# Optimization experiments

Measured on AMD Instinct MI355X. Metric: run time of the kernel, lower is better.

The kernel has to match this reference:

```python
import jax, jax.numpy as jnp
import numpy as np
from functools import partial

B = 1024          # batch of VRP instances
N_CUST = 100      # customers
N = N_CUST + 1    # nodes incl. depot (node 0)
E = 128           # embed_dim
H = 8             # n_heads
DH = E // H       # head depth
CLIP = 10.0
T = 2 * N         # fixed number of decode steps (env.n_nodes * 2)


def setup_inputs() -> dict:
    key = jax.random.key(0)
    ks = jax.random.split(key, 11)
    s = E ** -0.5
    return {
        "depot_xy": jax.random.uniform(ks[0], (B, 2), dtype=jnp.float32),
        "customer_xy": jax.random.uniform(ks[1], (B, N_CUST, 2), dtype=jnp.float32),
        # demands normalized by vehicle capacity (1..9 / 50 for VRP100)
        "demand": jax.random.uniform(ks[2], (B, N_CUST), dtype=jnp.float32, minval=0.02, maxval=0.18),
        "node_embeddings": jax.random.normal(ks[3], (B, N, E), dtype=jnp.float32),
        "graph_embedding": jax.random.normal(ks[4], (B, E), dtype=jnp.float32),
        "Wk1": jax.random.normal(ks[5], (E, E), dtype=jnp.float32) * s,
        "Wv": jax.random.normal(ks[6], (E, E), dtype=jnp.float32) * s,
        "Wk2": jax.random.normal(ks[7], (E, E), dtype=jnp.float32) * s,
        "Wq_fixed": jax.random.normal(ks[8], (E, E), dtype=jnp.float32) * s,
        "Wout": jax.random.normal(ks[9], (E, E), dtype=jnp.float32) * s,
        "Wq_step": jax.random.normal(ks[10], (E + 1, E), dtype=jnp.float32) * s,
    }


def _decode(depot_xy, customer_xy, demand, node_embeddings, graph_embedding,
            Wk1, Wv, Wk2, Wq_fixed, Wout, Wq_step):
    # ---- compute_static ----
    Q_fixed = jnp.einsum('be,ef->bf', graph_embedding, Wq_fixed)[:, None, :]  # [B,1,E]
    K1 = jnp.einsum('bne,ef->bnf', node_embeddings, Wk1)                      # [B,N,E]
    V  = jnp.einsum('bne,ef->bnf', node_embeddings, Wv)
    K2 = jnp.einsum('bne,ef->bnf', node_embeddings, Wk2)
    K1h = K1.reshape(B, N, H, DH)
    Vh  = V.reshape(B, N, H, DH)
    inv_sqrt_dh = 1.0 / np.sqrt(DH)
    inv_sqrt_e = 1.0 / np.sqrt(E)
    bidx = jnp.arange(B)
    NEG = jnp.float32(-1e9)

    def step(carry, _):
        mask, D, prev_node, visited = carry
        # step_context = [embedding of current node, remaining capacity D]
        prev_emb = node_embeddings[bidx, prev_node]                 # [B,E]
        step_context = jnp.concatenate([prev_emb, D], axis=-1)[:, None, :]  # [B,1,E+1]
        # ---- compute_dynamic ----
        Q1 = Q_fixed + jnp.einsum('bqc,cf->bqf', step_context, Wq_step)      # [B,1,E]
        Q1h = Q1.reshape(B, 1, H, DH)
        scores = jnp.einsum('bqhd,bkhd->bhqk', Q1h, K1h) * inv_sqrt_dh       # [B,H,1,N]
        scores = jnp.where(mask[:, None, None, :], NEG, scores)
        attn = jax.nn.softmax(scores, axis=-1)
        glimpse = jnp.einsum('bhqk,bkhd->bqhd', attn, Vh).reshape(B, 1, E)
        Q2 = jnp.einsum('bqe,ef->bqf', glimpse, Wout)                        # [B,1,E]
        logits = CLIP * jnp.tanh(jnp.einsum('bqe,bke->bqk', Q2, K2) * inv_sqrt_e)
        logits = jnp.where(mask[:, None, :], NEG, logits)[:, 0]             # [B,N]
        log_p = jax.nn.log_softmax(logits, axis=-1)
        next_node = jnp.argmax(log_p, axis=-1)                               # greedy decode
        # ---- env._get_step ----
        is_depot = next_node == 0
        cust = jnp.clip(next_node - 1, 0, N_CUST - 1)
        sel_dem = jnp.where(is_depot, 0.0, demand[bidx, cust])
        D_new = jnp.where(is_depot[:, None], 1.0, D - sel_dem[:, None])      # refill at depot
        sel_onehot = (jnp.arange(N_CUST)[None, :] == cust[:, None]) & (~is_depot[:, None])
        visited = visited | sel_onehot
        mask_cust = visited | (demand > D_new)                               # visited or too big
        all_visited = jnp.all(visited, axis=-1)
        mask_depot = is_depot & (~all_visited)                               # can't stay at depot
        mask = jnp.concatenate([mask_depot[:, None], mask_cust], axis=-1)
        return (mask, D_new, next_node, visited), (log_p, next_node)

    mask0 = jnp.concatenate([jnp.ones((B, 1), bool), jnp.zeros((B, N_CUST), bool)], axis=-1)
    D0 = jnp.ones((B, 1), jnp.float32)
    prev0 = jnp.zeros((B,), jnp.int32)
    visited0 = jnp.zeros((B, N_CUST), bool)
    _, (log_ps, tours) = jax.lax.scan(step, (mask0, D0, prev0, visited0), None, length=T)
    log_ps = jnp.transpose(log_ps, (1, 0, 2))   # [B,T,N]
    tours = jnp.transpose(tours, (1, 0))        # [B,T]

    # ---- get_costs ----
    coords = jnp.concatenate([depot_xy[:, None, :], customer_xy], axis=1)    # [B,N,2]
    d = coords[bidx[:, None], tours]                                         # [B,T,2]
    def seglen(v):
        return jnp.sqrt(jnp.sum(v * v, axis=-1) + 1e-10)
    cost = (seglen(d[:, 1:] - d[:, :-1]).sum(-1)
            + seglen(d[:, 0] - depot_xy) + seglen(d[:, -1] - depot_xy))
    # ---- get_log_likelihood ----
    ll = jnp.take_along_axis(log_ps, tours[..., None], axis=-1)[..., 0].sum(-1)
    return cost, ll


def reference(depot_xy, customer_xy, demand, node_embeddings, graph_embedding,
              Wk1, Wv, Wk2, Wq_fixed, Wout, Wq_step):
    return _decode(depot_xy, customer_xy, demand, node_embeddings, graph_embedding,
                   Wk1, Wv, Wk2, Wq_fixed, Wout, Wq_step)
```

## Files before the change

### kernel.cpp

```cpp
#include <hip/hip_runtime.h>
#include <math.h>

#define B_   1024
#define NC   100
#define NN   101
#define E_   128
#define T_   202
#define NEGV   -1.0e9
#define GAPTHR 1.0e-3f
#define INVSQE 0.08838834764831845f
#define INVSQED 0.08838834764831845

__device__ __forceinline__ float rdlane(float v, int l) {
    return __int_as_float(__builtin_amdgcn_readlane(__float_as_int(v), l));
}

__global__ void k_weights(const float* __restrict__ Wk2,
                          const float* __restrict__ Wout,
                          double* __restrict__ M64,
                          float* __restrict__ M32) {
    int g = blockIdx.x;
    int e = threadIdx.x;
    const float* w2 = Wk2 + g * E_;
    const float* wo = Wout + e * E_;
    double acc = 0.0;
#pragma unroll 8
    for (int f = 0; f < E_; ++f) acc += (double)w2[f] * (double)wo[f];
    M64[g * E_ + e] = acc;
    M32[g * E_ + e] = (float)acc;
}

__global__ __launch_bounds__(512, 2)
void k_decode(const float* __restrict__ depot_xy,
              const float* __restrict__ customer_xy,
              const float* __restrict__ demand,
              const float* __restrict__ node_emb,
              const float* __restrict__ graph_emb,
              const float* __restrict__ Wk1,
              const float* __restrict__ Wv,
              const float* __restrict__ Wq_fixed,
              const float* __restrict__ Wq_step,
              const double* __restrict__ M64,
              const float* __restrict__ M32,
              float* __restrict__ out)
{
    __shared__ float  sKs[NN * E_];
    __shared__ float  sV [NN * E_];
    __shared__ double sU[2224];
    __shared__ double sQfix64[E_];
    __shared__ double sWqD64[E_];
    __shared__ float  sQfix32[E_];
    __shared__ float  sWqD32[E_];
    __shared__ float  sInvS[8];
    __shared__ float  sCoord[2 * NN];
    __shared__ float  sDem[NC];
    __shared__ float  sD;
    __shared__ double sCost, sLL;
    __shared__ float  sPosX, sPosY;
    __shared__ int    sPrev, sMaskDepot, sTrig, sOvf;
    __shared__ unsigned long long sVis0, sVis1;

    float* fSc   = (float*)sU;
    float* fPart = (float*)sU + 832;
    float* fPx   = (float*)sU + 1344;
    double* dUZ = sU;
    double* dSc = sU + 1024;
    double* dQ1 = sU + 1832;
    double* dGl = sU + 1960;
    double* dVg = sU + 2088;

    const int b      = blockIdx.x;
    const int tid    = threadIdx.x;
    const int lane   = tid & 63;
    const int h      = __builtin_amdgcn_readfirstlane(tid >> 6);
    const int k1     = lane + 64;
    const int k_lane = tid & 127;
    const int q2u    = __builtin_amdgcn_readfirstlane(tid >> 7);
    const int e0     = q2u * 32;
    const int kb     = q2u * 26;

    const float* emb = node_emb + (size_t)b * NN * E_;

    if (tid < E_) {
        const float* ge = graph_emb + (size_t)b * E_;
        double acc = 0.0;
        for (int g = 0; g < E_; ++g)
            acc += (double)ge[g] * (double)Wq_fixed[g * E_ + tid];
        sQfix64[tid] = acc;
        sQfix32[tid] = (float)acc;
        sWqD64[tid]  = (double)Wq_step[128 * E_ + tid];
        sWqD32[tid]  = Wq_step[128 * E_ + tid];
    }
    if (tid < 2 * NN) {
        int k = tid >> 1, xy = tid & 1;
        sCoord[tid] = (k == 0) ? depot_xy[(size_t)b * 2 + xy]
                               : customer_xy[((size_t)b * NC + (k - 1)) * 2 + xy];
    }
    if (tid < NC) sDem[tid] = demand[(size_t)b * NC + tid];
    if (tid == 0) {
        sD = 1.f; sPrev = 0; sVis0 = 0ull; sVis1 = 0ull;
        sMaskDepot = 1; sCost = 0.0; sLL = 0.0; sTrig = 0; sOvf = 0;
        sPosX = depot_xy[(size_t)b * 2 + 0];
        sPosY = depot_xy[(size_t)b * 2 + 1];
    }

    for (int idx = tid; idx < NN * 32; idx += 512) {
        int k  = idx >> 5;
        int e4 = (idx & 31) * 4;
        const float* er = emb + (size_t)k * E_;
        float4 aV = {0.f, 0.f, 0.f, 0.f};
        float4 aK = {0.f, 0.f, 0.f, 0.f};
        for (int g = 0; g < E_; ++g) {
            float eg = er[g];
            float4 wv = *(const float4*)(Wv      + (size_t)g * E_ + e4);
            float4 wq = *(const float4*)(Wq_step + (size_t)g * E_ + e4);
            aV.x += eg * wv.x; aV.y += eg * wv.y;
            aV.z += eg * wv.z; aV.w += eg * wv.w;
            aK.x += eg * wq.x; aK.y += eg * wq.y;
            aK.z += eg * wq.z; aK.w += eg * wq.w;
        }
        *(float4*)(sV  + (size_t)k * E_ + e4) = aV;
        *(float4*)(sKs + (size_t)k * E_ + e4) = aK;
    }

    float rA[32];
#pragma unroll
    for (int j = 0; j < 32; ++j) rA[j] = 0.f;
    {
        const float* er0 = emb + (size_t)lane * E_;
        const float* er1 = emb + (size_t)((k1 < NN) ? k1 : lane) * E_;
        const float  e1s = (k1 < NN) ? 1.f : 0.f;
        const float* w1b = Wk1 + h * 16;
        for (int g = 0; g < E_; ++g) {
            float a0 = er0[g];
            float a1 = er1[g] * e1s;
            const float* w1 = w1b + (size_t)g * E_;
#pragma unroll
            for (int d = 0; d < 16; ++d) {
                rA[d]      += a0 * w1[d];
                rA[16 + d] += a1 * w1[d];
            }
        }
    }

    float rK2[32];
#pragma unroll
    for (int j = 0; j < 32; ++j) rK2[j] = 0.f;
    if (k_lane < NN) {
        const float* er = emb + (size_t)k_lane * E_;
        for (int g = 0; g < E_; ++g) {
            float eg = er[g];
            const float* mm = M32 + (size_t)g * E_ + e0;
#pragma unroll
            for (int j = 0; j < 32; ++j) rK2[j] += eg * mm[j];
        }
    }
    __syncthreads();

    for (int t = 0; t < T_; ++t) {
        {
            int prev = sPrev;
            float Dv = sD;
            int d_ = h * 16 + (lane & 15);
            float q1v = (sQfix32[d_] + sKs[(size_t)prev * E_ + d_]
                         + Dv * sWqD32[d_]) * 0.25f;

            unsigned long long v0 = sVis0, v1 = sVis1;
            bool mk0, mk1;
            if (lane == 0) mk0 = (sMaskDepot != 0);
            else {
                int c = lane - 1;
                mk0 = ((v0 >> c) & 1ull) || (sDem[c] > Dv);
            }
            if (k1 < NN) {
                int c = k1 - 1;
                bool vis = (c < 64) ? ((v0 >> c) & 1ull)
                                    : ((v1 >> (c - 64)) & 1ull);
                mk1 = vis || (sDem[c] > Dv);
            } else mk1 = true;

            float s0 = 0.f, s1 = 0.f;
#pragma unroll
            for (int d = 0; d < 16; ++d) {
                float qd = rdlane(q1v, d);
                s0 += rA[d] * qd;
                s1 += rA[16 + d] * qd;
            }
            bool ovf = (!mk0 && s0 > 80.f) || (!mk1 && s1 > 80.f);
            if (__any(ovf)) { if (lane == 0) sOvf = 1; }
            float w0 = mk0 ? 0.f : expf(fminf(s0, 80.f));
            float w1 = mk1 ? 0.f : expf(fminf(s1, 80.f));
            fSc[h * 104 + lane] = w0;
            if (k1 < 104) fSc[h * 104 + k1] = w1;
            float wsum = w0 + w1;
#pragma unroll
            for (int m = 32; m >= 1; m >>= 1) wsum += __shfl_xor(wsum, m);
            if (lane == 0) sInvS[h] = 1.0f / wsum;
        }
        __syncthreads();

        {
            int e = k_lane, hh = e >> 4;
            const float* sc = fSc + hh * 104 + kb;
            const float* vv = sV + (size_t)kb * E_ + e;
            float p = 0.f;
#pragma unroll
            for (int j = 0; j < 26; ++j) p += sc[j] * vv[j * E_];
            fPart[q2u * E_ + e] = p;
        }
        __syncthreads();

        {
            int ee = e0 + (tid & 31);
            float glv = (fPart[ee] + fPart[128 + ee] + fPart[256 + ee]
                         + fPart[384 + ee]) * sInvS[ee >> 4];
            float x = 0.f;
#pragma unroll
            for (int j = 0; j < 32; ++j) x += rK2[j] * rdlane(glv, j);
            if (k_lane < NN) fPx[q2u * E_ + k_lane] = x;
        }
        __syncthreads();

        if (tid < 64) {
            int kA = tid, kB = tid + 64;
            float xA = (fPx[kA] + fPx[128 + kA] + fPx[256 + kA] + fPx[384 + kA]) * INVSQE;
            bool mk1;
            if (kA == 0) mk1 = (sMaskDepot != 0);
            else {
                int c = kA - 1;
                bool vis = (c < 64) ? ((sVis0 >> c) & 1ull) : ((sVis1 >> (c - 64)) & 1ull);
                mk1 = vis || (sDem[c] > sD);
            }
            float xB = -3.0e38f; bool mk2 = true;
            if (kB < NN) {
                xB = (fPx[kB] + fPx[128 + kB] + fPx[256 + kB] + fPx[384 + kB]) * INVSQE;
                int c = kB - 1;
                bool vis = (c < 64) ? ((sVis0 >> c) & 1ull) : ((sVis1 >> (c - 64)) & 1ull);
                mk2 = vis || (sDem[c] > sD);
            }
            float a1v = mk1 ? -3.0e38f : xA;
            float a2v = mk2 ? -3.0e38f : xB;
            float m1, m2; int mi;
            if (a2v > a1v) { m1 = a2v; m2 = a1v; mi = kB; }
            else           { m1 = a1v; m2 = a2v; mi = kA; }
            float ls = 0.f;
            if (!mk1)              ls += expf(10.f * tanhf(xA));
            if (kB < NN && !mk2)   ls += expf(10.f * tanhf(xB));
#pragma unroll
            for (int off = 32; off > 0; off >>= 1) {
                float om1 = __shfl_xor(m1, off);
                float om2 = __shfl_xor(m2, off);
                float os  = __shfl_xor(ls, off);
                int   omi = __shfl_xor(mi, off);
                ls += os;
                if (om1 > m1 || (om1 == m1 && omi < mi)) {
                    m2 = fmaxf(m1, om2); m1 = om1; mi = omi;
                } else {
                    m2 = fmaxf(m2, om1);
                }
            }
            if (tid == 0) {
                float gap = m1 - m2;
                bool trig = !(gap >= GAPTHR) || (sOvf != 0);
                sOvf = 0;
                if (trig) {
                    sTrig = 1;
                } else {
                    float lsel = 10.f * tanhf(m1);
                    float logp = lsel - logf(ls);
                    int nxt = mi;
                    sLL += (double)logp;
                    bool isdep = (nxt == 0);
                    if (isdep) {
                        sD = 1.0f;
                    } else {
                        int c = nxt - 1;
                        sD = sD - sDem[c];
                        if (c < 64) sVis0 |= (1ull << c);
                        else        sVis1 |= (1ull << (c - 64));
                    }
                    bool allv = (sVis0 == 0xFFFFFFFFFFFFFFFFull) &&
                                (sVis1 == 0x0000000FFFFFFFFFull);
                    sMaskDepot = (isdep && !allv) ? 1 : 0;
                    sPrev = nxt;
                    float cx = sCoord[2 * nxt], cy = sCoord[2 * nxt + 1];
                    double dx = (double)cx - (double)sPosX;
                    double dy = (double)cy - (double)sPosY;
                    sCost += sqrt(dx * dx + dy * dy + 1e-10);
                    sPosX = cx; sPosY = cy;
                }
            }
        }
        __syncthreads();

        if (sTrig) {
            if (tid < E_) {
                const float* ep = emb + (size_t)sPrev * E_;
                double ks = 0.0;
                for (int g = 0; g < E_; ++g)
                    ks += (double)ep[g] * (double)Wq_step[(size_t)g * E_ + tid];
                dQ1[tid] = (sQfix64[tid] + ks + (double)sD * sWqD64[tid]) * 0.25;
            }
            __syncthreads();
            for (int idx = tid; idx < 1024; idx += 512) {
                int g = idx >> 3, hh = idx & 7;
                double u = 0.0;
#pragma unroll 4
                for (int d = 0; d < 16; ++d)
                    u += dQ1[hh * 16 + d] * (double)Wk1[(size_t)g * E_ + hh * 16 + d];
                dUZ[idx] = u;
            }
            __syncthreads();
            for (int idx = tid; idx < 1024; idx += 512) {
                int k = idx & 127, hh = idx >> 7;
                if (k < NN) {
                    bool mk;
                    if (k == 0) mk = (sMaskDepot != 0);
                    else {
                        int c = k - 1;
                        bool vis = (c < 64) ? ((sVis0 >> c) & 1ull) : ((sVis1 >> (c - 64)) & 1ull);
                        mk = vis || (sDem[c] > sD);
                    }
                    if (mk) dSc[hh * NN + k] = NEGV;
                    else {
                        const float* ek = emb + (size_t)k * E_;
                        double s = 0.0;
                        for (int g = 0; g < E_; ++g)
                            s += (double)ek[g] * dUZ[g * 8 + hh];
                        dSc[hh * NN + k] = s;
                    }
                }
            }
            __syncthreads();
            {
                int hh = tid >> 6, ln = tid & 63;
                int kA = ln, kB = ln + 64;
                double v1 = dSc[hh * NN + kA];
                double v2 = (kB < NN) ? dSc[hh * NN + kB] : -1.0e300;
                double m = fmax(v1, v2);
#pragma unroll
                for (int off = 32; off > 0; off >>= 1)
                    m = fmax(m, __shfl_xor(m, off));
                double e1 = exp(v1 - m);
                double e2 = (kB < NN) ? exp(v2 - m) : 0.0;
                double s = e1 + e2;
#pragma unroll
                for (int off = 32; off > 0; off >>= 1)
                    s += __shfl_xor(s, off);
                double inv = 1.0 / s;
                dSc[hh * NN + kA] = e1 * inv;
                if (kB < NN) dSc[hh * NN + kB] = e2 * inv;
            }
            __syncthreads();
            for (int idx = tid; idx < 1024; idx += 512) {
                int g = idx >> 3, hh = idx & 7;
                double z = 0.0;
                for (int k = 0; k < NN; ++k)
                    z += dSc[hh * NN + k] * (double)emb[(size_t)k * E_ + g];
                dUZ[idx] = z;
            }
            __syncthreads();
            if (tid < E_) {
                int hh = tid >> 4;
                double g2 = 0.0;
                for (int g = 0; g < E_; ++g)
                    g2 += dUZ[g * 8 + hh] * (double)Wv[(size_t)g * E_ + tid];
                dGl[tid] = g2;
            }
            __syncthreads();
            if (tid < E_) {
                double v = 0.0;
                for (int e = 0; e < E_; ++e)
                    v += dGl[e] * M64[(size_t)tid * E_ + e];
                dVg[tid] = v;
            }
            __syncthreads();
            if (tid < NN) {
                const float* ek = emb + (size_t)tid * E_;
                double x = 0.0;
                for (int g = 0; g < E_; ++g)
                    x += (double)ek[g] * dVg[g];
                dQ1[tid] = x * INVSQED;
            }
            __syncthreads();
            if (tid < 64) {
                int kA = tid, kB = tid + 64;
                double x1 = dQ1[kA];
                bool mk1;
                if (kA == 0) mk1 = (sMaskDepot != 0);
                else {
                    int c = kA - 1;
                    bool vis = (c < 64) ? ((sVis0 >> c) & 1ull) : ((sVis1 >> (c - 64)) & 1ull);
                    mk1 = vis || (sDem[c] > sD);
                }
                double x2 = 0.0; bool mk2 = true;
                if (kB < NN) {
                    x2 = dQ1[kB];
                    int c = kB - 1;
                    bool vis = (c < 64) ? ((sVis0 >> c) & 1ull) : ((sVis1 >> (c - 64)) & 1ull);
                    mk2 = vis || (sDem[c] > sD);
                }
                double a1 = mk1 ? -1.0e300 : x1;
                double a2 = (kB < NN && !mk2) ? x2 : -1.0e300;
                double mv; int mi;
                if (a1 >= a2) { mv = a1; mi = kA; } else { mv = a2; mi = kB; }
#pragma unroll
                for (int off = 32; off > 0; off >>= 1) {
                    double ov = __shfl_xor(mv, off);
                    int    oi = __shfl_xor(mi, off);
                    if (ov > mv || (ov == mv && oi < mi)) { mv = ov; mi = oi; }
                }
                double lmax = 10.0 * tanh(mv);
                double l1 = mk1 ? NEGV : 10.0 * tanh(x1);
                double l2 = (kB < NN) ? (mk2 ? NEGV : 10.0 * tanh(x2)) : 0.0;
                double s = exp(l1 - lmax) + ((kB < NN) ? exp(l2 - lmax) : 0.0);
#pragma unroll
                for (int off = 32; off > 0; off >>= 1)
                    s += __shfl_xor(s, off);
                if (tid == 0) {
                    int nxt = mi;
                    sLL += -log(s);
                    bool isdep = (nxt == 0);
                    if (isdep) {
                        sD = 1.0f;
                    } else {
                        int c = nxt - 1;
                        sD = sD - sDem[c];
                        if (c < 64) sVis0 |= (1ull << c);
                        else        sVis1 |= (1ull << (c - 64));
                    }
                    bool allv = (sVis0 == 0xFFFFFFFFFFFFFFFFull) &&
                                (sVis1 == 0x0000000FFFFFFFFFull);
                    sMaskDepot = (isdep && !allv) ? 1 : 0;
                    sPrev = nxt;
                    float cx = sCoord[2 * nxt], cy = sCoord[2 * nxt + 1];
                    double dx = (double)cx - (double)sPosX;
                    double dy = (double)cy - (double)sPosY;
                    sCost += sqrt(dx * dx + dy * dy + 1e-10);
                    sPosX = cx; sPosY = cy;
                    sTrig = 0;
                }
            }
            __syncthreads();
        }
    }

    if (tid == 0) {
        double dx = (double)sCoord[0] - (double)sPosX;
        double dy = (double)sCoord[1] - (double)sPosY;
        out[b]      = (float)(sCost + sqrt(dx * dx + dy * dy + 1e-10));
        out[B_ + b] = (float)sLL;
    }
}

extern "C" void kernel_launch(void* const* d_in, const int* in_sizes, int n_in,
                              void* d_out, int out_size, void* d_ws, size_t ws_size,
                              hipStream_t stream) {
    const float* depot = (const float*)d_in[0];
    const float* cust  = (const float*)d_in[1];
    const float* dem   = (const float*)d_in[2];
    const float* nemb  = (const float*)d_in[3];
    const float* gemb  = (const float*)d_in[4];
    const float* Wk1   = (const float*)d_in[5];
    const float* Wv    = (const float*)d_in[6];
    const float* Wk2   = (const float*)d_in[7];
    const float* Wqf   = (const float*)d_in[8];
    const float* Wout  = (const float*)d_in[9];
    const float* Wqs   = (const float*)d_in[10];
    float*  out = (float*)d_out;
    double* M64 = (double*)d_ws;
    float*  M32 = (float*)((char*)d_ws + 131072);

    k_weights<<<dim3(128), dim3(128), 0, stream>>>(Wk2, Wout, M64, M32);
    k_decode <<<dim3(B_),  dim3(512), 0, stream>>>(depot, cust, dem, nemb, gemb,
                                                   Wk1, Wv, Wqf, Wqs, M64, M32, out);
}
```

Baseline: 3.577 ms.

## Fuse per-head attention-value product into score wave and use fast intrinsics

New measurement: 3.171 ms. 11.3% less time.

```diff
diff --git a/kernel.cpp b/kernel.cpp
--- a/kernel.cpp
+++ b/kernel.cpp
@@ -13,6 +13,11 @@
 
 __device__ __forceinline__ float rdlane(float v, int l) {
     return __int_as_float(__builtin_amdgcn_readlane(__float_as_int(v), l));
+}
+__device__ __forceinline__ float fast_tanh(float x) {
+    float xc = fminf(fmaxf(x, -15.f), 15.f);
+    float e  = __expf(2.f * xc);
+    return (e - 1.f) / (e + 1.f);
 }
 
 __global__ void k_weights(const float* __restrict__ Wk2,
@@ -51,7 +56,6 @@
     __shared__ double sWqD64[E_];
     __shared__ float  sQfix32[E_];
     __shared__ float  sWqD32[E_];
-    __shared__ float  sInvS[8];
     __shared__ float  sCoord[2 * NN];
     __shared__ float  sDem[NC];
     __shared__ float  sD;
@@ -60,9 +64,9 @@
     __shared__ int    sPrev, sMaskDepot, sTrig, sOvf;
     __shared__ unsigned long long sVis0, sVis1;
 
-    float* fSc   = (float*)sU;
-    float* fPart = (float*)sU + 832;
-    float* fPx   = (float*)sU + 1344;
+    float* fSc = (float*)sU;
+    float* gl  = (float*)sU + 832;
+    float* fPx = (float*)sU + 960;
     double* dUZ = sU;
     double* dSc = sU + 1024;
     double* dQ1 = sU + 1832;
@@ -77,7 +81,6 @@
     const int k_lane = tid & 127;
     const int q2u    = __builtin_amdgcn_readfirstlane(tid >> 7);
     const int e0     = q2u * 32;
-    const int kb     = q2u * 26;
 
     const float* emb = node_emb + (size_t)b * NN * E_;
 
@@ -179,45 +182,60 @@
                 mk1 = vis || (sDem[c] > Dv);
             } else mk1 = true;
 
-            float s0 = 0.f, s1 = 0.f;
-#pragma unroll
-            for (int d = 0; d < 16; ++d) {
+            float s0a = 0.f, s0b = 0.f, s1a = 0.f, s1b = 0.f;
+#pragma unroll
+            for (int d = 0; d < 8; ++d) {
                 float qd = rdlane(q1v, d);
-                s0 += rA[d] * qd;
-                s1 += rA[16 + d] * qd;
-            }
+                s0a += rA[d] * qd;
+                s1a += rA[16 + d] * qd;
+            }
+#pragma unroll
+            for (int d = 8; d < 16; ++d) {
+                float qd = rdlane(q1v, d);
+                s0b += rA[d] * qd;
+                s1b += rA[16 + d] * qd;
+            }
+            float s0 = s0a + s0b, s1 = s1a + s1b;
             bool ovf = (!mk0 && s0 > 80.f) || (!mk1 && s1 > 80.f);
             if (__any(ovf)) { if (lane == 0) sOvf = 1; }
-            float w0 = mk0 ? 0.f : expf(fminf(s0, 80.f));
-            float w1 = mk1 ? 0.f : expf(fminf(s1, 80.f));
+            float w0 = mk0 ? 0.f : __expf(fminf(s0, 80.f));
+            float w1 = mk1 ? 0.f : __expf(fminf(s1, 80.f));
             fSc[h * 104 + lane] = w0;
             if (k1 < 104) fSc[h * 104 + k1] = w1;
-            float wsum = w0 + w1;
-#pragma unroll
-            for (int m = 32; m >= 1; m >>= 1) wsum += __shfl_xor(wsum, m);
-            if (lane == 0) sInvS[h] = 1.0f / wsum;
-        }
-        __syncthreads();
-
-        {
-            int e = k_lane, hh = e >> 4;
-            const float* sc = fSc + hh * 104 + kb;
-            const float* vv = sV + (size_t)kb * E_ + e;
-            float p = 0.f;
-#pragma unroll
-            for (int j = 0; j < 26; ++j) p += sc[j] * vv[j * E_];
-            fPart[q2u * E_ + e] = p;
+
+            __builtin_amdgcn_wave_barrier();
+
+            int cq4 = lane >> 4;
+            const float* sc = fSc + h * 104 + cq4 * 26;
+            const float* vv = sV + (size_t)(cq4 * 26) * E_ + d_;
+            float p = 0.f, ssum = 0.f;
+#pragma unroll
+            for (int j = 0; j < 26; ++j) {
+                float wgt = sc[j];
+                p    += wgt * vv[(size_t)j * E_];
+                ssum += wgt;
+            }
+            p    += __shfl_xor(p, 16);
+            ssum += __shfl_xor(ssum, 16);
+            p    += __shfl_xor(p, 32);
+            ssum += __shfl_xor(ssum, 32);
+            if (lane < 16) gl[d_] = p * (1.0f / ssum);
         }
         __syncthreads();
 
         {
             int ee = e0 + (tid & 31);
-            float glv = (fPart[ee] + fPart[128 + ee] + fPart[256 + ee]
-                         + fPart[384 + ee]) * sInvS[ee >> 4];
-            float x = 0.f;
-#pragma unroll
-            for (int j = 0; j < 32; ++j) x += rK2[j] * rdlane(glv, j);
-            if (k_lane < NN) fPx[q2u * E_ + k_lane] = x;
+            float glv = gl[ee];
+            float xa = 0.f, xb = 0.f, xc = 0.f, xd = 0.f;
+#pragma unroll
+            for (int j = 0; j < 8; ++j)   xa += rK2[j] * rdlane(glv, j);
+#pragma unroll
+            for (int j = 8; j < 16; ++j)  xb += rK2[j] * rdlane(glv, j);
+#pragma unroll
+            for (int j = 16; j < 24; ++j) xc += rK2[j] * rdlane(glv, j);
+#pragma unroll
+            for (int j = 24; j < 32; ++j) xd += rK2[j] * rdlane(glv, j);
+            if (k_lane < NN) fPx[q2u * E_ + k_lane] = (xa + xb) + (xc + xd);
         }
         __syncthreads();
 
@@ -240,34 +258,31 @@
             }
             float a1v = mk1 ? -3.0e38f : xA;
             float a2v = mk2 ? -3.0e38f : xB;
-            float m1, m2; int mi;
-            if (a2v > a1v) { m1 = a2v; m2 = a1v; mi = kB; }
-            else           { m1 = a1v; m2 = a2v; mi = kA; }
+            float m1; int mi;
+            if (a2v > a1v) { m1 = a2v; mi = kB; }
+            else           { m1 = a1v; mi = kA; }
             float ls = 0.f;
-            if (!mk1)              ls += expf(10.f * tanhf(xA));
-            if (kB < NN && !mk2)   ls += expf(10.f * tanhf(xB));
+            if (!mk1)              ls += __expf(10.f * fast_tanh(xA));
+            if (kB < NN && !mk2)   ls += __expf(10.f * fast_tanh(xB));
 #pragma unroll
             for (int off = 32; off > 0; off >>= 1) {
                 float om1 = __shfl_xor(m1, off);
-                float om2 = __shfl_xor(m2, off);
-                float os  = __shfl_xor(ls, off);
                 int   omi = __shfl_xor(mi, off);
-                ls += os;
-                if (om1 > m1 || (om1 == m1 && omi < mi)) {
-                    m2 = fmaxf(m1, om2); m1 = om1; mi = omi;
-                } else {
-                    m2 = fmaxf(m2, om1);
-                }
-            }
+                ls += __shfl_xor(ls, off);
+                if (om1 > m1 || (om1 == m1 && omi < mi)) { m1 = om1; mi = omi; }
+            }
+            bool near = false;
+            if (!mk1 && kA != mi && a1v > m1 - GAPTHR) near = true;
+            if (!mk2 && kB != mi && a2v > m1 - GAPTHR) near = true;
+            bool trigAny = __any(near);
             if (tid == 0) {
-                float gap = m1 - m2;
-                bool trig = !(gap >= GAPTHR) || (sOvf != 0);
+                bool trig = trigAny || (sOvf != 0) || !(m1 == m1);
                 sOvf = 0;
                 if (trig) {
                     sTrig = 1;
                 } else {
-                    float lsel = 10.f * tanhf(m1);
-                    float logp = lsel - logf(ls);
+                    float lsel = 10.f * fast_tanh(m1);
+                    float logp = lsel - __logf(ls);
                     int nxt = mi;
                     sLL += (double)logp;
                     bool isdep = (nxt == 0);
```
